# Performance work log

Hardware: AMD Instinct MI355X
Metric: run time of the kernel (lower is better)

## Reference

```python
import jax, jax.numpy as jnp
import numpy as np

N = 20000      # nodes
G = 400        # distinct TCR group ids
D_IN, H1, H2, D_OUT = 128, 256, 256, 128
LN_EPS = 1e-5


def _init_linear(key, fan_in, fan_out):
    s = 1.0 / np.sqrt(fan_in)
    return jax.random.uniform(key, (fan_in, fan_out), jnp.float32, -s, s)


def setup_inputs() -> dict:
    key = jax.random.key(0)
    ks = jax.random.split(key, 6)
    x = jax.random.normal(ks[0], (N, D_IN), jnp.float32)
    idx_TCR = jax.random.randint(ks[1], (N,), 0, G, dtype=jnp.int64)
    W1 = _init_linear(ks[2], D_IN, H1)
    W2 = _init_linear(ks[3], H1, H2)
    W3 = _init_linear(ks[4], H2, D_OUT)
    b1 = jnp.zeros((H1,), jnp.float32)
    b2 = jnp.zeros((H2,), jnp.float32)
    b3 = jnp.zeros((D_OUT,), jnp.float32)
    gamma = jnp.ones((D_OUT,), jnp.float32)
    beta = jnp.zeros((D_OUT,), jnp.float32)
    return {"x": x, "idx_TCR": idx_TCR, "W1": W1, "b1": b1,
            "W2": W2, "b2": b2, "W3": W3, "b3": b3,
            "gamma": gamma, "beta": beta}


def _build_edges(idx_TCR):
    # construct_graph: connect node pairs with equal idx, upper triangle only
    # (directed src<tgt edges, as in the torch code), then append self-loops
    # as PyG GCNConv.gcn_norm does.
    idx = np.asarray(idx_TCR).reshape(-1)
    n = idx.shape[0]
    eq = idx[:, None] == idx[None, :]
    src, tgt = np.nonzero(np.triu(eq, k=1))
    loop = np.arange(n)
    row = jnp.asarray(np.concatenate([src, loop]))  # message source
    col = jnp.asarray(np.concatenate([tgt, loop]))  # message target
    return row, col, n


def _gcn_norm(row, col, n, dtype):
    # degree from incoming edges (incl. self-loops), symmetric normalization
    deg = jax.ops.segment_sum(jnp.ones(row.shape[0], dtype), col, num_segments=n)
    dis = jnp.where(deg > 0, jax.lax.rsqrt(deg), jnp.zeros_like(deg))
    return dis[row] * dis[col]  # [E]


def _gcn_conv(x, W, b, row, col, norm, n):
    h = x @ W                                   # [N, out]
    msg = h[row] * norm[:, None]                # gather + scale, [E, out]
    out = jax.ops.segment_sum(msg, col, num_segments=n)  # scatter-add
    return out + b


def reference(x, idx_TCR, W1, b1, W2, b2, W3, b3, gamma, beta):
    row, col, n = _build_edges(idx_TCR)
    norm = _gcn_norm(row, col, n, x.dtype)
    h = jax.nn.relu(_gcn_conv(x, W1, b1, row, col, norm, n))
    h = jax.nn.relu(_gcn_conv(h, W2, b2, row, col, norm, n))
    h = jax.nn.relu(_gcn_conv(h, W3, b3, row, col, norm, n))
    # LayerNorm over last dim
    mu = h.mean(axis=-1, keepdims=True)
    var = ((h - mu) ** 2).mean(axis=-1, keepdims=True)
    return (h - mu) * jax.lax.rsqrt(var + LN_EPS) * gamma + beta
```

## Files before the change

kernel.cpp:

```cpp
#include <hip/hip_runtime.h>
#include <hip/hip_bf16.h>

#define NN 20000
#define NG 400
#define D_IN 128
#define H1 256
#define H2 256
#define D_OUT 128
#define NB_RANK ((NN + 255) / 256)
#define NB_PAD 80
#define WT_ELEMS (D_IN * H1 + H1 * H2 + H2 * D_OUT)

typedef __attribute__((ext_vector_type(8))) short short8;
typedef __attribute__((ext_vector_type(4))) short short4v;
typedef __attribute__((ext_vector_type(4))) float floatx4;

__device__ __forceinline__ short f2b(float f) {
    __hip_bfloat16 h = __float2bfloat16(f);
    return *(short*)&h;
}

__device__ __forceinline__ void gl_lds16(const void* g, void* l) {
    __builtin_amdgcn_global_load_lds(
        (__attribute__((address_space(1))) void*)g,
        (__attribute__((address_space(3))) void*)l, 16, 0, 0);
}


__global__ __launch_bounds__(256) void rank1_kernel(
    const int* __restrict__ idx, int* __restrict__ lrank,
    int* __restrict__ blockhist)
{
    __shared__ int sg[256];
    __shared__ int hist[NG];
    int t = threadIdx.x;
    int b = blockIdx.x;
    int j = b * 256 + t;
    for (int g = t; g < NG; g += 256) hist[g] = 0;
    int g = (j < NN) ? idx[j] : -1;
    sg[t] = g;
    __syncthreads();
    if (g >= 0) atomicAdd(&hist[g], 1);
    int r = 0;
    for (int s = 0; s < t; ++s) {
        if (sg[s] == g) r++;
    }
    __syncthreads();
    if (j < NN) lrank[j] = r;
    for (int gg = t; gg < NG; gg += 256) blockhist[gg * NB_PAD + b] = hist[gg];
}

__global__ __launch_bounds__(512) void rank2_kernel(
    const int* __restrict__ blockhist, int* __restrict__ blockoff,
    int* __restrict__ gs)
{
    __shared__ int tot[512];
    int g = threadIdx.x;
    int run = 0;
    if (g < NG) {
        int4 buf[NB_PAD / 4];
        const int4* src = (const int4*)(blockhist + g * NB_PAD);
#pragma unroll
        for (int i = 0; i < NB_PAD / 4; ++i) buf[i] = src[i];
        const int* bi = (const int*)buf;
#pragma unroll
        for (int b = 0; b < NB_RANK; ++b) {
            blockoff[g * NB_PAD + b] = run;
            run += bi[b];
        }
    }
    tot[threadIdx.x] = (g < NG) ? run : 0;
    __syncthreads();
#pragma unroll
    for (int off = 1; off < 512; off <<= 1) {
        int v = (threadIdx.x >= off) ? tot[threadIdx.x - off] : 0;
        __syncthreads();
        tot[threadIdx.x] += v;
        __syncthreads();
    }
    if (threadIdx.x == 0) gs[0] = 0;
    if (threadIdx.x < NG) gs[threadIdx.x + 1] = tot[threadIdx.x];
}

__global__ __launch_bounds__(256) void rank3_kernel(
    const int* __restrict__ idx, const int* __restrict__ lrank,
    const int* __restrict__ blockoff, const int* __restrict__ gs,
    float* __restrict__ dis, int* __restrict__ perm)
{
    int j = blockIdx.x * 256 + threadIdx.x;
    if (j >= NN) return;
    int g = idx[j];
    int r = blockoff[g * NB_PAD + blockIdx.x] + lrank[j];
    dis[j] = rsqrtf((float)(r + 1));
    perm[gs[g] + r] = j;
}


__global__ __launch_bounds__(256) void wt_all(
    const float* __restrict__ W1, const float* __restrict__ W2,
    const float* __restrict__ W3, __hip_bfloat16* __restrict__ Wt1,
    __hip_bfloat16* __restrict__ Wt2, __hip_bfloat16* __restrict__ Wt3)
{
    int o = blockIdx.x * 256 + threadIdx.x;
    if (o < D_IN * H1) {
        int n = o / D_IN, k = o - n * D_IN;
        Wt1[o] = __float2bfloat16(W1[(size_t)k * H1 + n]);
    } else if (o < D_IN * H1 + H1 * H2) {
        int p = o - D_IN * H1;
        int n = p / H1, k = p - n * H1;
        Wt2[p] = __float2bfloat16(W2[(size_t)k * H2 + n]);
    } else if (o < WT_ELEMS) {
        int p = o - D_IN * H1 - H1 * H2;
        int n = p / H2, k = p - n * H2;
        Wt3[p] = __float2bfloat16(W3[(size_t)k * D_OUT + n]);
    }
}


#define ST1 72
#define SA1 136
#define ST2 72
#define SA2 264
#define SH2 264
#define ST3 72
#define SF 132

__global__ __launch_bounds__(512) void fused_gcn(
    const float* __restrict__ x,
    const __hip_bfloat16* __restrict__ Wt1_,
    const __hip_bfloat16* __restrict__ Wt2_,
    const __hip_bfloat16* __restrict__ Wt3_,
    const float* __restrict__ b1, const float* __restrict__ b2,
    const float* __restrict__ b3,
    const float* __restrict__ gamma, const float* __restrict__ beta,
    const float* __restrict__ dis, const int* __restrict__ perm,
    const int* __restrict__ gs,
    float* __restrict__ out)
{
    __shared__ __align__(16) char RA[36864];
    __shared__ __align__(16) char RB[36864];
    __shared__ __align__(16) float b2s[256];
    __shared__ __align__(16) float b3s[128];
    __shared__ __align__(16) float sd[64];
    __shared__ int sp[64];

    float* XR = (float*)RA;
    short* T2 = (short*)RA;
    short* HB = (short*)RA;
    float* F  = (float*)RA;
    short* T1 = (short*)RB;
    short* A1 = (short*)(RB + 18432);
    short* A2 = (short*)RB;
    short* T3 = (short*)RB;

    int tid = threadIdx.x;
    int w = tid >> 6;
    int lane = tid & 63;
    int quad = lane >> 4;
    int l15 = lane & 15;

    int g = blockIdx.x;
    int s = gs[g], cnt = gs[g + 1] - s;
    if (cnt <= 0) return;

    if (tid < 256) b2s[tid] = b2[tid];
    if (tid < 128) b3s[tid] = b3[tid];

    float bj1[2];
#pragma unroll
    for (int nt = 0; nt < 2; ++nt) bj1[nt] = b1[(w * 2 + nt) * 16 + l15];
    float2 gmv = *(const float2*)&gamma[lane * 2];
    float2 btv = *(const float2*)&beta[lane * 2];

    auto ltfrag = [&](int nt, int k2) -> short8 {
        int thr = nt * 16 + l15 - k2 * 32 - quad * 8;
        short8 f;
#pragma unroll
        for (int e = 0; e < 8; ++e)
            f[e] = (e <= thr) ? (short)0x3F80 : (short)0;
        return f;
    };

    float c1[4], c2[2][4], c3[4];
#pragma unroll
    for (int r = 0; r < 4; ++r) {
        c1[r] = 0.f; c3[r] = 0.f;
        c2[0][r] = 0.f; c2[1][r] = 0.f;
    }

    const short* wt1p = (const short*)Wt1_;
    const short* wt2p = (const short*)Wt2_;
    const short* wt3p = (const short*)Wt3_;

    for (int base = 0; base < cnt; base += 64) {
        asm("" : "+s"(wt1p), "+s"(wt2p), "+s"(wt3p));

        int mt = min(64, cnt - base);
        __syncthreads();
        if (tid < 64) {
            int p = (tid < mt) ? perm[s + base + tid] : perm[s];
            sp[tid] = p;
            sd[tid] = (tid < mt) ? dis[p] : 0.0f;
        }
        __syncthreads();

        float djn[4];
#pragma unroll
        for (int nt = 0; nt < 4; ++nt) djn[nt] = sd[nt * 16 + l15];

        {
            int r0 = 8 * w;
#pragma unroll
            for (int ii = 0; ii < 4; ++ii) {
                int row = r0 + 2 * ii + (lane >> 5);
                const float* src = x + (size_t)sp[row] * D_IN + (lane & 31) * 4;
                gl_lds16(src, &XR[(r0 + 2 * ii) * D_IN]);
            }
        }
        __syncthreads();

        {
            int c = tid & 127;
            int q = tid >> 7;
#pragma unroll
            for (int p = 0; p < 2; ++p) {
                int rb = q * 16 + p * 8;
                short8 o;
#pragma unroll
                for (int e = 0; e < 8; ++e)
                    o[e] = f2b(XR[(rb + e) * D_IN + c] * sd[rb + e]);
                *(short8*)&T1[c * ST1 + rb] = o;
            }
        }
        __syncthreads();

        {
            floatx4 acc[4];
#pragma unroll
            for (int nt = 0; nt < 4; ++nt) acc[nt] = (floatx4)0.0f;
#pragma unroll
            for (int k2 = 0; k2 < 2; ++k2) {
                short8 af = *(const short8*)&T1[(w * 16 + l15) * ST1 + k2 * 32 + quad * 8];
#pragma unroll
                for (int nt = 0; nt < 4; ++nt)
                    acc[nt] = __builtin_amdgcn_mfma_f32_16x16x32_bf16(
                        af, ltfrag(nt, k2), acc[nt], 0, 0, 0);
            }
            float nc[4] = {0.f, 0.f, 0.f, 0.f};
#pragma unroll
            for (int nt = 0; nt < 4; ++nt) {
                float tmp[4];
#pragma unroll
                for (int r = 0; r < 4; ++r) tmp[r] = acc[nt][r] + c1[r];
                if (nt == 3) {
#pragma unroll
                    for (int r = 0; r < 4; ++r) nc[r] = tmp[r];
                }
                short4v o4;
#pragma unroll
                for (int r = 0; r < 4; ++r) o4[r] = f2b(tmp[r] * djn[nt]);
                *(short4v*)&A1[(nt * 16 + l15) * SA1 + w * 16 + quad * 4] = o4;
            }
#pragma unroll
            for (int r = 0; r < 4; ++r)
                c1[r] = __shfl(nc[r], (lane & 48) + 15);
        }
        __syncthreads();

        {
            floatx4 acc[4][2];
#pragma unroll
            for (int i = 0; i < 4; ++i)
#pragma unroll
                for (int nt = 0; nt < 2; ++nt) acc[i][nt] = (floatx4)0.0f;
#pragma unroll
            for (int kk = 0; kk < 4; ++kk) {
                short8 af[4], bf[2];
#pragma unroll
                for (int i = 0; i < 4; ++i)
                    af[i] = *(const short8*)&A1[(i * 16 + l15) * SA1 + kk * 32 + quad * 8];
#pragma unroll
                for (int nt = 0; nt < 2; ++nt)
                    bf[nt] = *(const short8*)&wt1p[((size_t)(w * 2 + nt) * 16 + l15) * D_IN + kk * 32 + quad * 8];
#pragma unroll
                for (int i = 0; i < 4; ++i)
#pragma unroll
                    for (int nt = 0; nt < 2; ++nt)
                        acc[i][nt] = __builtin_amdgcn_mfma_f32_16x16x32_bf16(
                            af[i], bf[nt], acc[i][nt], 0, 0, 0);
            }
#pragma unroll
            for (int i = 0; i < 4; ++i) {
                float4 sdv = *(const float4*)&sd[i * 16 + quad * 4];
#pragma unroll
                for (int nt = 0; nt < 2; ++nt) {
                    short4v o4;
                    o4[0] = f2b(fmaxf(acc[i][nt][0] + bj1[nt], 0.0f) * sdv.x);
                    o4[1] = f2b(fmaxf(acc[i][nt][1] + bj1[nt], 0.0f) * sdv.y);
                    o4[2] = f2b(fmaxf(acc[i][nt][2] + bj1[nt], 0.0f) * sdv.z);
                    o4[3] = f2b(fmaxf(acc[i][nt][3] + bj1[nt], 0.0f) * sdv.w);
                    *(short4v*)&T2[((w * 2 + nt) * 16 + l15) * ST2 + i * 16 + quad * 4] = o4;
                }
            }
        }
        __syncthreads();

        {
            floatx4 acc[2][4];
#pragma unroll
            for (int i = 0; i < 2; ++i)
#pragma unroll
                for (int nt = 0; nt < 4; ++nt) acc[i][nt] = (floatx4)0.0f;
#pragma unroll
            for (int k2 = 0; k2 < 2; ++k2) {
                short8 af[2];
#pragma unroll
                for (int i = 0; i < 2; ++i)
                    af[i] = *(const short8*)&T2[((2 * w + i) * 16 + l15) * ST2 + k2 * 32 + quad * 8];
#pragma unroll
                for (int nt = 0; nt < 4; ++nt) {
                    short8 lt = ltfrag(nt, k2);
#pragma unroll
                    for (int i = 0; i < 2; ++i)
                        acc[i][nt] = __builtin_amdgcn_mfma_f32_16x16x32_bf16(
                            af[i], lt, acc[i][nt], 0, 0, 0);
                }
            }
#pragma unroll
            for (int i = 0; i < 2; ++i) {
                float nc[4] = {0.f, 0.f, 0.f, 0.f};
#pragma unroll
                for (int nt = 0; nt < 4; ++nt) {
                    float tmp[4];
#pragma unroll
                    for (int r = 0; r < 4; ++r) tmp[r] = acc[i][nt][r] + c2[i][r];
                    if (nt == 3) {
#pragma unroll
                        for (int r = 0; r < 4; ++r) nc[r] = tmp[r];
                    }
                    short4v o4;
#pragma unroll
                    for (int r = 0; r < 4; ++r) o4[r] = f2b(tmp[r] * djn[nt]);
                    *(short4v*)&A2[(nt * 16 + l15) * SA2 + (2 * w + i) * 16 + quad * 4] = o4;
                }
#pragma unroll
                for (int r = 0; r < 4; ++r)
                    c2[i][r] = __shfl(nc[r], (lane & 48) + 15);
            }
        }
        __syncthreads();

        {
            floatx4 acc[2][4];
#pragma unroll
            for (int i = 0; i < 2; ++i)
#pragma unroll
                for (int nt = 0; nt < 4; ++nt) acc[i][nt] = (floatx4)0.0f;
#pragma unroll
            for (int kk = 0; kk < 8; ++kk) {
                short8 af[2], bf[4];
#pragma unroll
                for (int i = 0; i < 2; ++i)
                    af[i] = *(const short8*)&wt2p[((size_t)(2 * w + i) * 16 + l15) * H1 + kk * 32 + quad * 8];
#pragma unroll
                for (int nt = 0; nt < 4; ++nt)
                    bf[nt] = *(const short8*)&A2[(nt * 16 + l15) * SA2 + kk * 32 + quad * 8];
#pragma unroll
                for (int i = 0; i < 2; ++i)
#pragma unroll
                    for (int nt = 0; nt < 4; ++nt)
                        acc[i][nt] = __builtin_amdgcn_mfma_f32_16x16x32_bf16(
                            af[i], bf[nt], acc[i][nt], 0, 0, 0);
            }
#pragma unroll
            for (int i = 0; i < 2; ++i) {
                float4 bb = *(const float4*)&b2s[(2 * w + i) * 16 + quad * 4];
#pragma unroll
                for (int nt = 0; nt < 4; ++nt) {
                    short4v o4;
                    o4[0] = f2b(fmaxf(acc[i][nt][0] + bb.x, 0.0f));
                    o4[1] = f2b(fmaxf(acc[i][nt][1] + bb.y, 0.0f));
                    o4[2] = f2b(fmaxf(acc[i][nt][2] + bb.z, 0.0f));
                    o4[3] = f2b(fmaxf(acc[i][nt][3] + bb.w, 0.0f));
                    *(short4v*)&HB[(nt * 16 + l15) * SH2 + (2 * w + i) * 16 + quad * 4] = o4;
                }
            }
        }
        __syncthreads();

        {
            floatx4 acc[4];
#pragma unroll
            for (int i = 0; i < 4; ++i) acc[i] = (floatx4)0.0f;
#pragma unroll
            for (int kk = 0; kk < 8; ++kk) {
                short8 bf = *(const short8*)&wt3p[((size_t)w * 16 + l15) * H2 + kk * 32 + quad * 8];
#pragma unroll
                for (int i = 0; i < 4; ++i) {
                    short8 af = *(const short8*)&HB[(i * 16 + l15) * SH2 + kk * 32 + quad * 8];
                    acc[i] = __builtin_amdgcn_mfma_f32_16x16x32_bf16(
                        af, bf, acc[i], 0, 0, 0);
                }
            }
#pragma unroll
            for (int i = 0; i < 4; ++i) {
                float4 sdv = *(const float4*)&sd[i * 16 + quad * 4];
                short4v o4;
                o4[0] = f2b(acc[i][0] * sdv.x);
                o4[1] = f2b(acc[i][1] * sdv.y);
                o4[2] = f2b(acc[i][2] * sdv.z);
                o4[3] = f2b(acc[i][3] * sdv.w);
                *(short4v*)&T3[(w * 16 + l15) * ST3 + i * 16 + quad * 4] = o4;
            }
        }
        __syncthreads();

        {
            floatx4 acc[4];
#pragma unroll
            for (int nt = 0; nt < 4; ++nt) acc[nt] = (floatx4)0.0f;
#pragma unroll
            for (int k2 = 0; k2 < 2; ++k2) {
                short8 af = *(const short8*)&T3[(w * 16 + l15) * ST3 + k2 * 32 + quad * 8];
#pragma unroll
                for (int nt = 0; nt < 4; ++nt)
                    acc[nt] = __builtin_amdgcn_mfma_f32_16x16x32_bf16(
                        af, ltfrag(nt, k2), acc[nt], 0, 0, 0);
            }
            float4 bb = *(const float4*)&b3s[w * 16 + quad * 4];
            float nc[4] = {0.f, 0.f, 0.f, 0.f};
#pragma unroll
            for (int nt = 0; nt < 4; ++nt) {
                float tmp[4];
#pragma unroll
                for (int r = 0; r < 4; ++r) tmp[r] = acc[nt][r] + c3[r];
                if (nt == 3) {
#pragma unroll
                    for (int r = 0; r < 4; ++r) nc[r] = tmp[r];
                }
                float4 o;
                o.x = fmaxf(tmp[0] * djn[nt] + bb.x, 0.0f);
                o.y = fmaxf(tmp[1] * djn[nt] + bb.y, 0.0f);
                o.z = fmaxf(tmp[2] * djn[nt] + bb.z, 0.0f);
                o.w = fmaxf(tmp[3] * djn[nt] + bb.w, 0.0f);
                *(float4*)&F[(nt * 16 + l15) * SF + w * 16 + quad * 4] = o;
            }
#pragma unroll
            for (int r = 0; r < 4; ++r)
                c3[r] = __shfl(nc[r], (lane & 48) + 15);
        }
        __syncthreads();

        for (int r = w; r < mt; r += 8) {
            float2 v = *(const float2*)&F[r * SF + lane * 2];
            float s1 = v.x + v.y;
            float s2v = v.x * v.x + v.y * v.y;
#pragma unroll
            for (int off = 32; off > 0; off >>= 1) {
                s1 += __shfl_down(s1, off);
                s2v += __shfl_down(s2v, off);
            }
            s1 = __shfl(s1, 0);
            s2v = __shfl(s2v, 0);
            float mu = s1 * (1.0f / D_OUT);
            float var = s2v * (1.0f / D_OUT) - mu * mu;
            float rstd = rsqrtf(var + 1e-5f);
            float2 o;
            o.x = (v.x - mu) * rstd * gmv.x + btv.x;
            o.y = (v.y - mu) * rstd * gmv.y + btv.y;
            *(float2*)&out[(size_t)sp[r] * D_OUT + lane * 2] = o;
        }
    }
}


extern "C" void kernel_launch(void* const* d_in, const int* in_sizes, int n_in,
                              void* d_out, int out_size, void* d_ws, size_t ws_size,
                              hipStream_t stream) {
    const float* x     = (const float*)d_in[0];
    const int*   idx   = (const int*)d_in[1];
    const float* W1    = (const float*)d_in[2];
    const float* b1    = (const float*)d_in[3];
    const float* W2    = (const float*)d_in[4];
    const float* b2    = (const float*)d_in[5];
    const float* W3    = (const float*)d_in[6];
    const float* b3    = (const float*)d_in[7];
    const float* gamma = (const float*)d_in[8];
    const float* beta  = (const float*)d_in[9];
    float* out = (float*)d_out;

    char* ws = (char*)d_ws;
    size_t off = 0;
    auto alloc = [&](size_t bytes) -> void* {
        void* p = (void*)(ws + off);
        off += (bytes + 255) & ~(size_t)255;
        return p;
    };
    float* dis   = (float*)alloc(NN * sizeof(float));
    int*   perm  = (int*)alloc(NN * sizeof(int));
    int*   lrank = (int*)alloc(NN * sizeof(int));
    int*   gs    = (int*)alloc((NG + 1) * sizeof(int));
    int*   bhist = (int*)alloc(NG * NB_PAD * sizeof(int));
    int*   boff  = (int*)alloc(NG * NB_PAD * sizeof(int));
    __hip_bfloat16* Wt1 = (__hip_bfloat16*)alloc((size_t)D_IN * H1 * 2);
    __hip_bfloat16* Wt2 = (__hip_bfloat16*)alloc((size_t)H1 * H2 * 2);
    __hip_bfloat16* Wt3 = (__hip_bfloat16*)alloc((size_t)H2 * D_OUT * 2);

    rank1_kernel<<<NB_RANK, 256, 0, stream>>>(idx, lrank, bhist);
    rank2_kernel<<<1, 512, 0, stream>>>(bhist, boff, gs);
    rank3_kernel<<<NB_RANK, 256, 0, stream>>>(idx, lrank, boff, gs, dis, perm);
    wt_all<<<(WT_ELEMS + 255) / 256, 256, 0, stream>>>(
        W1, W2, W3, Wt1, Wt2, Wt3);

    fused_gcn<<<NG, 512, 0, stream>>>(
        x, Wt1, Wt2, Wt3, b1, b2, b3, gamma, beta, dis, perm, gs, out);
}
```

Baseline: 141.6 us.

## Fold group membership scan into fused GCN kernel, drop rank kernels

New measurement: 132.1 us. 6.7% less time.

```diff
diff --git a/kernel.cpp b/kernel.cpp
--- a/kernel.cpp
+++ b/kernel.cpp
@@ -7,9 +7,8 @@
 #define H1 256
 #define H2 256
 #define D_OUT 128
-#define NB_RANK ((NN + 255) / 256)
-#define NB_PAD 80
 #define WT_ELEMS (D_IN * H1 + H1 * H2 + H2 * D_OUT)
+#define MCAP 1024
 
 typedef __attribute__((ext_vector_type(8))) short short8;
 typedef __attribute__((ext_vector_type(4))) short short4v;
@@ -24,75 +23,6 @@
     __builtin_amdgcn_global_load_lds(
         (__attribute__((address_space(1))) void*)g,
         (__attribute__((address_space(3))) void*)l, 16, 0, 0);
-}
-
-
-__global__ __launch_bounds__(256) void rank1_kernel(
-    const int* __restrict__ idx, int* __restrict__ lrank,
-    int* __restrict__ blockhist)
-{
-    __shared__ int sg[256];
-    __shared__ int hist[NG];
-    int t = threadIdx.x;
-    int b = blockIdx.x;
-    int j = b * 256 + t;
-    for (int g = t; g < NG; g += 256) hist[g] = 0;
-    int g = (j < NN) ? idx[j] : -1;
-    sg[t] = g;
-    __syncthreads();
-    if (g >= 0) atomicAdd(&hist[g], 1);
-    int r = 0;
-    for (int s = 0; s < t; ++s) {
-        if (sg[s] == g) r++;
-    }
-    __syncthreads();
-    if (j < NN) lrank[j] = r;
-    for (int gg = t; gg < NG; gg += 256) blockhist[gg * NB_PAD + b] = hist[gg];
-}
-
-__global__ __launch_bounds__(512) void rank2_kernel(
-    const int* __restrict__ blockhist, int* __restrict__ blockoff,
-    int* __restrict__ gs)
-{
-    __shared__ int tot[512];
-    int g = threadIdx.x;
-    int run = 0;
-    if (g < NG) {
-        int4 buf[NB_PAD / 4];
-        const int4* src = (const int4*)(blockhist + g * NB_PAD);
-#pragma unroll
-        for (int i = 0; i < NB_PAD / 4; ++i) buf[i] = src[i];
-        const int* bi = (const int*)buf;
-#pragma unroll
-        for (int b = 0; b < NB_RANK; ++b) {
-            blockoff[g * NB_PAD + b] = run;
-            run += bi[b];
-        }
-    }
-    tot[threadIdx.x] = (g < NG) ? run : 0;
-    __syncthreads();
-#pragma unroll
-    for (int off = 1; off < 512; off <<= 1) {
-        int v = (threadIdx.x >= off) ? tot[threadIdx.x - off] : 0;
-        __syncthreads();
-        tot[threadIdx.x] += v;
-        __syncthreads();
-    }
-    if (threadIdx.x == 0) gs[0] = 0;
-    if (threadIdx.x < NG) gs[threadIdx.x + 1] = tot[threadIdx.x];
-}
-
-__global__ __launch_bounds__(256) void rank3_kernel(
-    const int* __restrict__ idx, const int* __restrict__ lrank,
-    const int* __restrict__ blockoff, const int* __restrict__ gs,
-    float* __restrict__ dis, int* __restrict__ perm)
-{
-    int j = blockIdx.x * 256 + threadIdx.x;
-    if (j >= NN) return;
-    int g = idx[j];
-    int r = blockoff[g * NB_PAD + blockIdx.x] + lrank[j];
-    dis[j] = rsqrtf((float)(r + 1));
-    perm[gs[g] + r] = j;
 }
 
 
@@ -126,15 +56,13 @@
 #define SF 132
 
 __global__ __launch_bounds__(512) void fused_gcn(
-    const float* __restrict__ x,
+    const float* __restrict__ x, const int* __restrict__ idx,
     const __hip_bfloat16* __restrict__ Wt1_,
     const __hip_bfloat16* __restrict__ Wt2_,
     const __hip_bfloat16* __restrict__ Wt3_,
     const float* __restrict__ b1, const float* __restrict__ b2,
     const float* __restrict__ b3,
     const float* __restrict__ gamma, const float* __restrict__ beta,
-    const float* __restrict__ dis, const int* __restrict__ perm,
-    const int* __restrict__ gs,
     float* __restrict__ out)
 {
     __shared__ __align__(16) char RA[36864];
@@ -143,6 +71,8 @@
     __shared__ __align__(16) float b3s[128];
     __shared__ __align__(16) float sd[64];
     __shared__ int sp[64];
+    __shared__ int mlist[MCAP];
+    __shared__ int wcnt[8];
 
     float* XR = (float*)RA;
     short* T2 = (short*)RA;
@@ -158,9 +88,44 @@
     int lane = tid & 63;
     int quad = lane >> 4;
     int l15 = lane & 15;
-
     int g = blockIdx.x;
-    int s = gs[g], cnt = gs[g + 1] - s;
+
+    int llen = 0;
+    for (int B = 0; B < NN; B += 2048) {
+        int j0 = B + 4 * tid;
+        int4 v = make_int4(-1, -1, -1, -1);
+        if (j0 + 3 < NN) {
+            v = *(const int4*)&idx[j0];
+        } else {
+            if (j0 < NN)     v.x = idx[j0];
+            if (j0 + 1 < NN) v.y = idx[j0 + 1];
+            if (j0 + 2 < NN) v.z = idx[j0 + 2];
+        }
+        bool f0 = (v.x == g), f1 = (v.y == g), f2 = (v.z == g), f3 = (v.w == g);
+        unsigned long long m0 = __ballot(f0), m1 = __ballot(f1);
+        unsigned long long m2 = __ballot(f2), m3 = __ballot(f3);
+        unsigned long long lowm = (1ull << lane) - 1ull;
+        int p = __popcll(m0 & lowm) + __popcll(m1 & lowm) +
+                __popcll(m2 & lowm) + __popcll(m3 & lowm);
+        if (lane == 0)
+            wcnt[w] = __popcll(m0) + __popcll(m1) + __popcll(m2) + __popcll(m3);
+        __syncthreads();
+        int wbase = 0, tot = 0;
+        for (int ww = 0; ww < 8; ++ww) {
+            int c = wcnt[ww];
+            if (ww < w) wbase += c;
+            tot += c;
+        }
+        int s0 = llen + wbase + p;
+        int e0 = (int)f0, e1 = (int)f1, e2 = (int)f2;
+        if (f0 && s0 < MCAP)                mlist[s0] = j0;
+        if (f1 && s0 + e0 < MCAP)           mlist[s0 + e0] = j0 + 1;
+        if (f2 && s0 + e0 + e1 < MCAP)      mlist[s0 + e0 + e1] = j0 + 2;
+        if (f3 && s0 + e0 + e1 + e2 < MCAP) mlist[s0 + e0 + e1 + e2] = j0 + 3;
+        llen += tot;
+        __syncthreads();
+    }
+    int cnt = min(llen, MCAP);
     if (cnt <= 0) return;
 
     if (tid < 256) b2s[tid] = b2[tid];
@@ -198,9 +163,8 @@
         int mt = min(64, cnt - base);
         __syncthreads();
         if (tid < 64) {
-            int p = (tid < mt) ? perm[s + base + tid] : perm[s];
-            sp[tid] = p;
-            sd[tid] = (tid < mt) ? dis[p] : 0.0f;
+            sp[tid] = (tid < mt) ? mlist[base + tid] : mlist[0];
+            sd[tid] = (tid < mt) ? rsqrtf((float)(base + tid + 1)) : 0.0f;
         }
         __syncthreads();
 
@@ -496,22 +460,13 @@
         off += (bytes + 255) & ~(size_t)255;
         return p;
     };
-    float* dis   = (float*)alloc(NN * sizeof(float));
-    int*   perm  = (int*)alloc(NN * sizeof(int));
-    int*   lrank = (int*)alloc(NN * sizeof(int));
-    int*   gs    = (int*)alloc((NG + 1) * sizeof(int));
-    int*   bhist = (int*)alloc(NG * NB_PAD * sizeof(int));
-    int*   boff  = (int*)alloc(NG * NB_PAD * sizeof(int));
     __hip_bfloat16* Wt1 = (__hip_bfloat16*)alloc((size_t)D_IN * H1 * 2);
     __hip_bfloat16* Wt2 = (__hip_bfloat16*)alloc((size_t)H1 * H2 * 2);
     __hip_bfloat16* Wt3 = (__hip_bfloat16*)alloc((size_t)H2 * D_OUT * 2);
 
-    rank1_kernel<<<NB_RANK, 256, 0, stream>>>(idx, lrank, bhist);
-    rank2_kernel<<<1, 512, 0, stream>>>(bhist, boff, gs);
-    rank3_kernel<<<NB_RANK, 256, 0, stream>>>(idx, lrank, boff, gs, dis, perm);
     wt_all<<<(WT_ELEMS + 255) / 256, 256, 0, stream>>>(
         W1, W2, W3, Wt1, Wt2, Wt3);
 
     fused_gcn<<<NG, 512, 0, stream>>>(
-        x, Wt1, Wt2, Wt3, b1, b2, b3, gamma, beta, dis, perm, gs, out);
+        x, idx, Wt1, Wt2, Wt3, b1, b2, b3, gamma, beta, out);
 }
```
